# Kernel tuning notes

Measured on AMD Instinct MI355X. Metric: run time of the kernel, lower is better.

Reference implementation:

```python
import jax, jax.numpy as jnp
import numpy as np

N_NODES = 32768
N_EDGES = 131072
BATCH = 512
SEQ_LEN = 1000
VOCAB = 26  # vocab_size=25 + 1 padding row
EMB = 128


def _bn(x, g, b):
    # BatchNorm1d forward with batch statistics (training-mode math), eps=1e-5
    m = x.mean(0)
    v = x.var(0)
    return g * (x - m) * jax.lax.rsqrt(v + 1e-5) + b


def _gcn(x, src, dst, W, b, n):
    deg = 1.0 + jax.ops.segment_sum(jnp.ones(src.shape[0], x.dtype), dst, num_segments=n)
    dis = jax.lax.rsqrt(deg)
    xw = x @ W
    msg = xw[src] * (dis[src] * dis[dst])[:, None]
    agg = jax.ops.segment_sum(msg, dst, num_segments=n) + xw * (dis * dis)[:, None]
    return agg + b


def _conv1d(x, k, b, pad):
    # x: [B, C_in, L], k: [C_out, C_in, K]
    y = jax.lax.conv_general_dilated(x, k, (1,), [(pad, pad)],
                                     dimension_numbers=('NCH', 'OIH', 'NCH'))
    return y + b[None, :, None]


def setup_inputs() -> dict:
    key = jax.random.key(0)
    ks = jax.random.split(key, 32)
    f = lambda i, shape, s=0.1: (jax.random.normal(ks[i], shape, dtype=jnp.float32) * s)
    inp = {
        'x': jax.random.normal(ks[0], (N_NODES, 5), dtype=jnp.float32),
        'edge_index': jax.random.randint(ks[1], (2, N_EDGES), 0, N_NODES, dtype=jnp.int32),
        'batch': jnp.sort(jax.random.randint(ks[2], (N_NODES,), 0, BATCH, dtype=jnp.int32)),
        'protein_seq': jax.random.randint(ks[3], (BATCH, SEQ_LEN), 0, VOCAB, dtype=jnp.int32),
        # GCN weights
        'W1': f(4, (5, 64)), 'b1': f(5, (64,)),
        'g1': jnp.ones((64,)), 'bt1': jnp.zeros((64,)),
        'W2': f(6, (64, 128)), 'b2': f(7, (128,)),
        'g2': jnp.ones((128,)), 'bt2': jnp.zeros((128,)),
        'W3': f(8, (128, 128)), 'b3': f(9, (128,)),
        'g3': jnp.ones((128,)), 'bt3': jnp.zeros((128,)),
        # protein embedding (row 0 = padding_idx, zeroed)
        'emb': f(10, (VOCAB, EMB)).at[0].set(0.0),
        # protein convs
        'ck1': f(11, (32, 128, 4)), 'cb1': f(12, (32,)),
        'ck2': f(13, (64, 32, 6)), 'cb2': f(14, (64,)),
        'ck3': f(15, (96, 64, 8)), 'cb3': f(16, (96,)),
        'fw1': f(17, (224, 512)), 'fb1': f(18, (512,)),
        'fw2': f(19, (512, 256)), 'fb2': f(20, (256,)),
        'fw3': f(21, (256, 1)), 'fb3': f(22, (1,)),
    }
    return inp


def reference(x, edge_index, batch, protein_seq,
              W1, b1, g1, bt1, W2, b2, g2, bt2, W3, b3, g3, bt3,
              emb, ck1, cb1, ck2, cb2, ck3, cb3,
              fw1, fb1, fw2, fb2, fw3, fb3):
    src, dst = edge_index[0], edge_index[1]
    relu = jax.nn.relu
    # Drug GNN encoder
    h = relu(_bn(_gcn(x, src, dst, W1, b1, N_NODES), g1, bt1))
    h = relu(_bn(_gcn(h, src, dst, W2, b2, N_NODES), g2, bt2))
    h = relu(_bn(_gcn(h, src, dst, W3, b3, N_NODES), g3, bt3))
    cnt = jax.ops.segment_sum(jnp.ones(N_NODES, h.dtype), batch, num_segments=BATCH)
    drug_emb = jax.ops.segment_sum(h, batch, num_segments=BATCH) / jnp.maximum(cnt, 1.0)[:, None]
    # Protein CNN encoder
    e = emb[protein_seq]                    # [B, L, 128]
    p = jnp.transpose(e, (0, 2, 1))         # [B, 128, L]
    p = relu(_conv1d(p, ck1, cb1, 1))       # [B, 32, 999]
    p = relu(_conv1d(p, ck2, cb2, 2))       # [B, 64, 998]
    p = relu(_conv1d(p, ck3, cb3, 3))       # [B, 96, 997]
    prot_emb = p.max(axis=2)                # [B, 96]
    c = jnp.concatenate([drug_emb, prot_emb], axis=1)  # [B, 224]
    c = relu(c @ fw1 + fb1)
    c = relu(c @ fw2 + fb2)
    out = (c @ fw3 + fb3)[:, 0]             # [B]
    return out
```

## Files before the change

kernel.cpp:

```cpp
#include <hip/hip_runtime.h>

#define NN 32768
#define NE 131072
#define NB 512
#define SL 1000

using bf16x8 = __attribute__((ext_vector_type(8))) short;
using f32x4  = __attribute__((ext_vector_type(4))) float;

static __device__ __forceinline__ unsigned short f2b(float f) {
  union { float f; unsigned u; } x; x.f = f;
  unsigned r = x.u + 0x7fffu + ((x.u >> 16) & 1u);
  return (unsigned short)(r >> 16);
}

static __device__ __forceinline__ void bn_from_raw(float sum, float ssq, float g, float b,
                                                   float& sc, float& sh) {
  float m = sum / 32768.f;
  float v = ssq / 32768.f - m * m;
  sc = g * rsqrtf(v + 1e-5f);
  sh = b - m * sc;
}

__global__ void k_degprep(const int* __restrict__ dst, int* __restrict__ degi,
// ... 192 lines not shown
      acc[t].x += a.y * w1.x; acc[t].y += a.y * w1.y; acc[t].z += a.y * w1.z; acc[t].w += a.y * w1.w;
      acc[t].x += a.z * w2.x; acc[t].y += a.z * w2.y; acc[t].z += a.z * w2.z; acc[t].w += a.z * w2.w;
      acc[t].x += a.w * w3.x; acc[t].y += a.w * w3.y; acc[t].z += a.w * w3.z; acc[t].w += a.w * w3.w;
    }
  }
  float4 s4 = {0.f, 0.f, 0.f, 0.f}, ss4 = {0.f, 0.f, 0.f, 0.f};
#pragma unroll
  for (int t = 0; t < TN; ++t) {
    float4 o = acc[t];
    if (RELU) {
      o.x = fmaxf(o.x, 0.f); o.y = fmaxf(o.y, 0.f);
      o.z = fmaxf(o.z, 0.f); o.w = fmaxf(o.w, 0.f);
    }
    *(float4*)&out[(n0 + t) * C_OUT + co] = o;
    if (STATS) {
      s4.x += o.x; s4.y += o.y; s4.z += o.z; s4.w += o.w;
      ss4.x += o.x * o.x; ss4.y += o.y * o.y;
      ss4.z += o.z * o.z; ss4.w += o.w * o.w;
    }
  }
  if (STATS) {
    __shared__ float red2[GPB][C_OUT];
    int grp = threadIdx.x / CO4;
    *(float4*)&red2[grp][co] = s4;
    __syncthreads();
    if (threadIdx.x < C_OUT) {
      float t = 0.f;
#pragma unroll
      for (int s = 0; s < GPB; ++s) t += red2[s][threadIdx.x];
      atomicAdd(&st[threadIdx.x], t);
    }
    __syncthreads();
    *(float4*)&red2[grp][co] = ss4;
    __syncthreads();
    if (threadIdx.x < C_OUT) {
      float t = 0.f;
#pragma unroll
      for (int s = 0; s < GPB; ++s) t += red2[s][threadIdx.x];
      atomicAdd(&st[C_OUT + threadIdx.x], t);
    }
  }
}

__launch_bounds__(256)
__global__ void k_reg(const float* __restrict__ cbuf,
                      const float* __restrict__ fw1, const float* __restrict__ fb1,
                      const float* __restrict__ fw2, const float* __restrict__ fb2,
                      const float* __restrict__ fw3, const float* __restrict__ fb3,
                      float* __restrict__ out) {
  __shared__ float cin[224];
  __shared__ float h1[512];
  __shared__ float h2[256];
  __shared__ float red[4];
  int b = blockIdx.x, t = threadIdx.x;
  if (t < 224) cin[t] = cbuf[b * 224 + t];
  __syncthreads();
  {
    float a0 = fb1[t], a1 = fb1[t + 256];
    for (int ci = 0; ci < 224; ++ci) {
      float av = cin[ci];
      a0 += av * fw1[ci * 512 + t];
      a1 += av * fw1[ci * 512 + t + 256];
    }
    h1[t] = fmaxf(a0, 0.f);
    h1[t + 256] = fmaxf(a1, 0.f);
  }
  __syncthreads();
  {
    float a = fb2[t];
    for (int ci = 0; ci < 512; ++ci) a += h1[ci] * fw2[ci * 256 + t];
    h2[t] = fmaxf(a, 0.f);
  }
  __syncthreads();
  {
    float p = h2[t] * fw3[t];
#pragma unroll
    for (int off = 32; off > 0; off >>= 1) p += __shfl_down(p, off, 64);
    if ((t & 63) == 0) red[t >> 6] = p;
    __syncthreads();
    if (t == 0) out[b] = red[0] + red[1] + red[2] + red[3] + fb3[0];
  }
}

__launch_bounds__(256, 3)
__global__ void conv_mfma(const int* __restrict__ seq, const unsigned short* __restrict__ emb_bf,
                          const unsigned short* __restrict__ wt1g, const float* __restrict__ cb1,
                          const unsigned short* __restrict__ wt2g, const float* __restrict__ cb2,
                          const unsigned short* __restrict__ wt3g, const float* __restrict__ cb3,
                          const float* __restrict__ agg, const float* __restrict__ st3,
                          const float* __restrict__ g3, const float* __restrict__ bt3,
                          const int* __restrict__ batch, float* __restrict__ outmax) {
  __shared__ __align__(16) unsigned short s_w[12288];
  __shared__ __align__(16) unsigned short s_c1[4864];
  __shared__ __align__(16) unsigned short s_c2[9216];
  __shared__ int s_tok[152];
  __shared__ int s_max[96];

  int tid = threadIdx.x;
  int b = blockIdx.y;

  if (blockIdx.x == 8) {
    __shared__ int s_lo, s_hi;
    if (tid == 0) {
      int lo = 0, hi = NN;
      while (lo < hi) { int m = (lo + hi) >> 1; if (batch[m] < b) lo = m + 1; else hi = m; }
      s_lo = lo;
      hi = NN;
      while (lo < hi) { int m = (lo + hi) >> 1; if (batch[m] <= b) lo = m + 1; else hi = m; }
      s_hi = lo;
    }
    __syncthreads();
    if (tid < 128) {
      int lo = s_lo, hi = s_hi, c = tid;
      float sc, sh;
      bn_from_raw(st3[c], st3[128 + c], g3[c], bt3[c], sc, sh);
      float s = 0.f;
      for (int n = lo; n < hi; ++n) s += fmaxf(agg[(long)n * 128 + c] * sc + sh, 0.f);
      outmax[b * 224 + c] = s / fmaxf((float)(hi - lo), 1.0f);
    }
    return;
  }

  int t0 = blockIdx.x * 128;

  if (tid < 96) s_max[tid] = 0;
  if (tid < 152) {
    int p = t0 - 6 + tid;
    s_tok[tid] = (p >= 0 && p < SL) ? seq[b * SL + p] : 0;
  }
  if (tid < 128) ((int*)(s_c1 + 144 * 32))[tid] = 0;

  {
    int v0 = tid, v1 = tid + 256;
    *(bf16x8*)&s_w[(v0 >> 4) * 128 + ((((v0 >> 4) ^ v0) & 15) << 3)] = *(const bf16x8*)(wt1g + v0 * 8);
    *(bf16x8*)&s_w[(v1 >> 4) * 128 + ((((v1 >> 4) ^ v1) & 15) << 3)] = *(const bf16x8*)(wt1g + v1 * 8);
  }
  __syncthreads();

  int lane = tid & 63, wave = tid >> 6;
  int l15 = lane & 15, quad = lane >> 4;

  {
    int mt0 = wave, mt1 = wave + 4;
    f32x4 acc0[2], acc1[2], acc2[2];
#pragma unroll
    for (int nt = 0; nt < 2; ++nt) {
      float bv = cb1[nt * 16 + l15];
      acc0[nt] = (f32x4){bv, bv, bv, bv};
      acc1[nt] = (f32x4){bv, bv, bv, bv};
      acc2[nt] = (f32x4){bv, bv, bv, bv};
    }
    for (int kt = 0; kt < 4; ++kt) {
      int bo = (kt & 1) * 4096;
      if (kt < 3) {
        int bo2 = 4096 - bo;
        const unsigned short* wsrc = wt1g + (kt + 1) * 4096;
        int v0 = tid, v1 = tid + 256;
        *(bf16x8*)&s_w[bo2 + (v0 >> 4) * 128 + ((((v0 >> 4) ^ v0) & 15) << 3)] = *(const bf16x8*)(wsrc + v0 * 8);
        *(bf16x8*)&s_w[bo2 + (v1 >> 4) * 128 + ((((v1 >> 4) ^ v1) & 15) << 3)] = *(const bf16x8*)(wsrc + v1 * 8);
      }
      const unsigned short* e0 = emb_bf + s_tok[mt0 * 16 + l15 + kt] * 128 + quad * 8;
      const unsigned short* e1 = emb_bf + s_tok[mt1 * 16 + l15 + kt] * 128 + quad * 8;
#pragma unroll
      for (int cb = 0; cb < 4; ++cb) {
        bf16x8 a0 = *(const bf16x8*)(e0 + cb * 32);
        bf16x8 a1 = *(const bf16x8*)(e1 + cb * 32);
#pragma unroll
        for (int nt = 0; nt < 2; ++nt) {
          bf16x8 bf = *(const bf16x8*)&s_w[bo + (nt * 16 + l15) * 128 + (((cb * 4 + quad) ^ l15) << 3)];
          acc0[nt] = __builtin_amdgcn_mfma_f32_16x16x32_bf16(a0, bf, acc0[nt], 0, 0, 0);
          acc1[nt] = __builtin_amdgcn_mfma_f32_16x16x32_bf16(a1, bf, acc1[nt], 0, 0, 0);
        }
      }
      if (wave == 0) {
        const unsigned short* e2 = emb_bf + s_tok[128 + l15 + kt] * 128 + quad * 8;
#pragma unroll
        for (int cb = 0; cb < 4; ++cb) {
          bf16x8 a2 = *(const bf16x8*)(e2 + cb * 32);
#pragma unroll
          for (int nt = 0; nt < 2; ++nt) {
            bf16x8 bf = *(const bf16x8*)&s_w[bo + (nt * 16 + l15) * 128 + (((cb * 4 + quad) ^ l15) << 3)];
            acc2[nt] = __builtin_amdgcn_mfma_f32_16x16x32_bf16(a2, bf, acc2[nt], 0, 0, 0);
          }
        }
      }
      __syncthreads();
    }
#pragma unroll
    for (int nt = 0; nt < 2; ++nt) {
      int co = nt * 16 + l15;
#pragma unroll
      for (int r = 0; r < 4; ++r) {
        {
          int m = mt0 * 16 + quad * 4 + r;
          int l1 = t0 - 5 + m;
          unsigned short hv = f2b(fmaxf(acc0[nt][r], 0.f));
          s_c1[m * 32 + ((((co >> 3) ^ m) & 3) << 3) + (co & 7)] = (l1 >= 0 && l1 < 999) ? hv : (unsigned short)0;
        }
        {
          int m = mt1 * 16 + quad * 4 + r;
          int l1 = t0 - 5 + m;
          unsigned short hv = f2b(fmaxf(acc1[nt][r], 0.f));
          s_c1[m * 32 + ((((co >> 3) ^ m) & 3) << 3) + (co & 7)] = (l1 >= 0 && l1 < 999) ? hv : (unsigned short)0;
        }
      }
    }
    if (wave == 0) {
#pragma unroll
      for (int nt = 0; nt < 2; ++nt) {
        int co = nt * 16 + l15;
#pragma unroll
        for (int r = 0; r < 4; ++r) {
          int m = 128 + quad * 4 + r;
          int l1 = t0 - 5 + m;
          unsigned short hv = f2b(fmaxf(acc2[nt][r], 0.f));
          s_c1[m * 32 + ((((co >> 3) ^ m) & 3) << 3) + (co & 7)] = (l1 >= 0 && l1 < 999) ? hv : (unsigned short)0;
        }
      }
    }
  }

  {
    bf16x8 w2t[6];
#pragma unroll
    for (int c = 0; c < 6; ++c) w2t[c] = *(const bf16x8*)(wt2g + (c * 256 + tid) * 8);
#pragma unroll
    for (int c = 0; c < 6; ++c) {
      int ch = c * 256 + tid;
      int row = ch >> 2;
      *(bf16x8*)&s_w[row * 32 + (((row ^ ch) & 3) << 3)] = w2t[c];
    }
    __syncthreads();
  }

  {
    int mt0 = wave, mt1 = wave + 4;
    f32x4 acc[2][4];
#pragma unroll
    for (int nt = 0; nt < 4; ++nt) {
      float bv = cb2[nt * 16 + l15];
      acc[0][nt] = (f32x4){bv, bv, bv, bv};
      acc[1][nt] = (f32x4){bv, bv, bv, bv};
    }
    for (int kt = 0; kt < 6; ++kt) {
      int r0 = mt0 * 16 + l15 + kt, r1 = mt1 * 16 + l15 + kt;
      bf16x8 a0 = *(const bf16x8*)&s_c1[r0 * 32 + (((quad ^ r0) & 3) << 3)];
      bf16x8 a1 = *(const bf16x8*)&s_c1[r1 * 32 + (((quad ^ r1) & 3) << 3)];
#pragma unroll
      for (int nt = 0; nt < 4; ++nt) {
        int wr = kt * 64 + nt * 16 + l15;
        bf16x8 bf = *(const bf16x8*)&s_w[wr * 32 + (((quad ^ wr) & 3) << 3)];
        acc[0][nt] = __builtin_amdgcn_mfma_f32_16x16x32_bf16(a0, bf, acc[0][nt], 0, 0, 0);
        acc[1][nt] = __builtin_amdgcn_mfma_f32_16x16x32_bf16(a1, bf, acc[1][nt], 0, 0, 0);
      }
    }
#pragma unroll
    for (int mb = 0; mb < 2; ++mb) {
      int mt = mb ? mt1 : mt0;
#pragma unroll
      for (int nt = 0; nt < 4; ++nt) {
        int co = nt * 16 + l15;
#pragma unroll
        for (int r = 0; r < 4; ++r) {
          int m = mt * 16 + quad * 4 + r;
          int l2 = t0 - 3 + m;
          unsigned short hv = f2b(fmaxf(acc[mb][nt][r], 0.f));
          s_c2[m * 64 + ((((co >> 3) ^ m) & 7) << 3) + (co & 7)] = (l2 >= 0 && l2 < 998) ? hv : (unsigned short)0;
        }
      }
    }
    if (wave == 0) {
      f32x4 acc8[4];
#pragma unroll
      for (int nt = 0; nt < 4; ++nt) {
        float bv = cb2[nt * 16 + l15];
        acc8[nt] = (f32x4){bv, bv, bv, bv};
      }
      for (int kt = 0; kt < 6; ++kt) {
        int r0 = 128 + l15 + kt;
        bf16x8 a0 = *(const bf16x8*)&s_c1[r0 * 32 + (((quad ^ r0) & 3) << 3)];
#pragma unroll
        for (int nt = 0; nt < 4; ++nt) {
          int wr = kt * 64 + nt * 16 + l15;
          bf16x8 bf = *(const bf16x8*)&s_w[wr * 32 + (((quad ^ wr) & 3) << 3)];
          acc8[nt] = __builtin_amdgcn_mfma_f32_16x16x32_bf16(a0, bf, acc8[nt], 0, 0, 0);
        }
      }
#pragma unroll
      for (int nt = 0; nt < 4; ++nt) {
        int co = nt * 16 + l15;
#pragma unroll
        for (int r = 0; r < 4; ++r) {
          int m = 128 + quad * 4 + r;
          int l2 = t0 - 3 + m;
          unsigned short hv = f2b(fmaxf(acc8[nt][r], 0.f));
          s_c2[m * 64 + ((((co >> 3) ^ m) & 7) << 3) + (co & 7)] = (l2 >= 0 && l2 < 998) ? hv : (unsigned short)0;
        }
      }
    }
  }

  {
    bf16x8 w3t[3];
#pragma unroll
    for (int c = 0; c < 3; ++c) w3t[c] = *(const bf16x8*)(wt3g + (c * 256 + tid) * 8);
    __syncthreads();
#pragma unroll
    for (int c = 0; c < 3; ++c) {
      int ch = c * 256 + tid;
      int row = ch >> 3;
      *(bf16x8*)&s_w[row * 64 + (((row ^ ch) & 7) << 3)] = w3t[c];
    }
    __syncthreads();
  }

  {
    int mt0 = wave, mt1 = wave + 4;
    f32x4 acc[2][6];
#pragma unroll
    for (int nt = 0; nt < 6; ++nt) {
      float bv = cb3[nt * 16 + l15];
      acc[0][nt] = (f32x4){bv, bv, bv, bv};
      acc[1][nt] = (f32x4){bv, bv, bv, bv};
    }
    for (int kt = 0; kt < 8; ++kt) {
      bf16x8 w3t[3];
      if (kt < 7) {
#pragma unroll
        for (int c = 0; c < 3; ++c)
          w3t[c] = *(const bf16x8*)(wt3g + ((kt + 1) * 768 + c * 256 + tid) * 8);
      }
      int bo = (kt & 1) * 6144;
      int ra0 = mt0 * 16 + l15 + kt, ra1 = mt1 * 16 + l15 + kt;
#pragma unroll
      for (int cb = 0; cb < 2; ++cb) {
        bf16x8 a0 = *(const bf16x8*)&s_c2[ra0 * 64 + ((((cb * 4 + quad) ^ ra0) & 7) << 3)];
        bf16x8 a1 = *(const bf16x8*)&s_c2[ra1 * 64 + ((((cb * 4 + quad) ^ ra1) & 7) << 3)];
#pragma unroll
        for (int nt = 0; nt < 6; ++nt) {
          int wr = nt * 16 + l15;
          bf16x8 bf = *(const bf16x8*)&s_w[bo + wr * 64 + ((((cb * 4 + quad) ^ wr) & 7) << 3)];
          acc[0][nt] = __builtin_amdgcn_mfma_f32_16x16x32_bf16(a0, bf, acc[0][nt], 0, 0, 0);
          acc[1][nt] = __builtin_amdgcn_mfma_f32_16x16x32_bf16(a1, bf, acc[1][nt], 0, 0, 0);
        }
      }
      if (kt < 7) {
        int bo2 = 6144 - bo;
#pragma unroll
        for (int c = 0; c < 3; ++c) {
          int ch = c * 256 + tid;
          int row = ch >> 3;
          *(bf16x8*)&s_w[bo2 + row * 64 + (((row ^ ch) & 7) << 3)] = w3t[c];
        }
      }
      __syncthreads();
    }
#pragma unroll
    for (int nt = 0; nt < 6; ++nt) {
      int co = nt * 16 + l15;
      float mx = 0.f;
#pragma unroll
      for (int mb = 0; mb < 2; ++mb) {
        int mt = mb ? mt1 : mt0;
#pragma unroll
        for (int r = 0; r < 4; ++r) {
          int l3 = t0 + mt * 16 + quad * 4 + r;
          if (l3 < 997) mx = fmaxf(mx, acc[mb][nt][r]);
        }
      }
      atomicMax(&s_max[co], __float_as_int(mx));
    }
  }
  __syncthreads();
  if (tid < 96) atomicMax((int*)&outmax[b * 224 + 128 + tid], s_max[tid]);
}

extern "C" void kernel_launch(void* const* d_in, const int* in_sizes, int n_in,
                              void* d_out, int out_size, void* d_ws, size_t ws_size,
                              hipStream_t stream) {
  (void)in_sizes; (void)n_in; (void)out_size; (void)ws_size;
  const float* x = (const float*)d_in[0];
  const int* ei = (const int*)d_in[1];
  const int* batch = (const int*)d_in[2];
  const int* seq = (const int*)d_in[3];
  const float* W1 = (const float*)d_in[4];
  const float* g1 = (const float*)d_in[6];
  const float* bt1 = (const float*)d_in[7];
  const float* W2 = (const float*)d_in[8];
  const float* g2 = (const float*)d_in[10];
  const float* bt2 = (const float*)d_in[11];
  const float* W3 = (const float*)d_in[12];
  const float* g3 = (const float*)d_in[14];
  const float* bt3 = (const float*)d_in[15];
  const float* emb = (const float*)d_in[16];
  const float* ck1 = (const float*)d_in[17];
  const float* cb1 = (const float*)d_in[18];
  const float* ck2 = (const float*)d_in[19];
  const float* cb2 = (const float*)d_in[20];
  const float* ck3 = (const float*)d_in[21];
  const float* cb3 = (const float*)d_in[22];
  const float* fw1 = (const float*)d_in[23];
  const float* fb1 = (const float*)d_in[24];
  const float* fw2 = (const float*)d_in[25];
  const float* fb2 = (const float*)d_in[26];
  const float* fw3 = (const float*)d_in[27];
  const float* fb3 = (const float*)d_in[28];
  const int* src = ei;
  const int* dst = ei + NE;

  float* ws = (float*)d_ws;
  float* bufA = ws;
  float* bufB = ws + 4194304;
  float* dis = ws + 8388608;
  float* stats = ws + 8421376;
  float* cbuf = ws + 8422032;
  int* degi = (int*)(ws + 8536720);
  int* base = degi + NN;
  int* cursor = base + NN + 1;
  unsigned short* csr_src = (unsigned short*)(cursor + NN);
  unsigned short* emb_bf = (unsigned short*)(ws + 8700564);
  unsigned short* wt1 = emb_bf + 3328;
  unsigned short* wt2 = wt1 + 16384;
  unsigned short* wt3 = wt2 + 12288;
  float* out = (float*)d_out;

  hipMemsetAsync(stats, 0, (656 + 114688 + 32768) * sizeof(float), stream);

  k_degprep<<<NE / 256, 256, 0, stream>>>(dst, degi, emb, ck1, ck2, ck3, emb_bf, wt1, wt2, wt3);
  k_scan<<<1, 1024, 0, stream>>>(degi, base, cursor, dis);
  k_fill<<<NE / 256, 256, 0, stream>>>(src, dst, cursor, csr_src, NE);

  k_gfc1s<<<NN / 256, 256, 0, stream>>>(x, dis, base, csr_src, W1, bufA, stats);
  k_gbngather<64><<<NN * 16 / 256, 256, 0, stream>>>(bufA, dis, base, csr_src, stats, g1, bt1, bufB);
  k_fc4<128, 64, 4, false, false, true><<<1024, 256, 0, stream>>>(bufB, W2, nullptr, bufA, stats + 128, NN);
  k_gbngather<128><<<NN * 32 / 256, 256, 0, stream>>>(bufA, dis, base, csr_src, stats + 128, g2, bt2, bufB);
  k_fc4<128, 128, 4, false, false, true><<<1024, 256, 0, stream>>>(bufB, W3, nullptr, bufA, stats + 384, NN);

  conv_mfma<<<dim3(9, NB), 256, 0, stream>>>(seq, emb_bf, wt1, cb1, wt2, cb2, wt3, cb3,
                                             bufA, stats + 384, g3, bt3, batch, cbuf);

  k_reg<<<NB, 256, 0, stream>>>(cbuf, fw1, fb1, fw2, fb2, fw3, fb3, out);
}
```

Before: 431.2 us.

## Read conv weights directly from global memory instead of staging in LDS

Removes the 24 KB shared weight buffer and its double-buffered staging for all three conv layers, so MFMA B operands are loaded straight from global or L2 memory. This drops many __syncthreads and LDS writes, and the smaller LDS footprint lets launch bounds rise to 4 blocks per CU. The cost is more global-load latency inside the MFMA loops, since the weight reads now depend on cache hits, and possible register pressure under the tighter occupancy bound.

```diff
diff --git a/kernel.cpp b/kernel.cpp
--- a/kernel.cpp
+++ b/kernel.cpp
@@ -298,7 +298,7 @@
   }
 }
 
-__launch_bounds__(256, 3)
+__launch_bounds__(256, 4)
 __global__ void conv_mfma(const int* __restrict__ seq, const unsigned short* __restrict__ emb_bf,
                           const unsigned short* __restrict__ wt1g, const float* __restrict__ cb1,
                           const unsigned short* __restrict__ wt2g, const float* __restrict__ cb2,
@@ -306,7 +306,6 @@
                           const float* __restrict__ agg, const float* __restrict__ st3,
                           const float* __restrict__ g3, const float* __restrict__ bt3,
                           const int* __restrict__ batch, float* __restrict__ outmax) {
-  __shared__ __align__(16) unsigned short s_w[12288];
   __shared__ __align__(16) unsigned short s_c1[4864];
   __shared__ __align__(16) unsigned short s_c2[9216];
   __shared__ int s_tok[152];
@@ -345,12 +344,6 @@
     s_tok[tid] = (p >= 0 && p < SL) ? seq[b * SL + p] : 0;
   }
   if (tid < 128) ((int*)(s_c1 + 144 * 32))[tid] = 0;
-
-  {
-    int v0 = tid, v1 = tid + 256;
-    *(bf16x8*)&s_w[(v0 >> 4) * 128 + ((((v0 >> 4) ^ v0) & 15) << 3)] = *(const bf16x8*)(wt1g + v0 * 8);
-    *(bf16x8*)&s_w[(v1 >> 4) * 128 + ((((v1 >> 4) ^ v1) & 15) << 3)] = *(const bf16x8*)(wt1g + v1 * 8);
-  }
   __syncthreads();
 
   int lane = tid & 63, wave = tid >> 6;
@@ -367,23 +360,16 @@
       acc2[nt] = (f32x4){bv, bv, bv, bv};
     }
     for (int kt = 0; kt < 4; ++kt) {
-      int bo = (kt & 1) * 4096;
-      if (kt < 3) {
-        int bo2 = 4096 - bo;
-        const unsigned short* wsrc = wt1g + (kt + 1) * 4096;
-        int v0 = tid, v1 = tid + 256;
-        *(bf16x8*)&s_w[bo2 + (v0 >> 4) * 128 + ((((v0 >> 4) ^ v0) & 15) << 3)] = *(const bf16x8*)(wsrc + v0 * 8);
-        *(bf16x8*)&s_w[bo2 + (v1 >> 4) * 128 + ((((v1 >> 4) ^ v1) & 15) << 3)] = *(const bf16x8*)(wsrc + v1 * 8);
-      }
       const unsigned short* e0 = emb_bf + s_tok[mt0 * 16 + l15 + kt] * 128 + quad * 8;
       const unsigned short* e1 = emb_bf + s_tok[mt1 * 16 + l15 + kt] * 128 + quad * 8;
+      const unsigned short* wb = wt1g + kt * 4096 + l15 * 128 + quad * 8;
 #pragma unroll
       for (int cb = 0; cb < 4; ++cb) {
         bf16x8 a0 = *(const bf16x8*)(e0 + cb * 32);
         bf16x8 a1 = *(const bf16x8*)(e1 + cb * 32);
 #pragma unroll
         for (int nt = 0; nt < 2; ++nt) {
-          bf16x8 bf = *(const bf16x8*)&s_w[bo + (nt * 16 + l15) * 128 + (((cb * 4 + quad) ^ l15) << 3)];
+          bf16x8 bf = *(const bf16x8*)(wb + nt * 2048 + cb * 32);
           acc0[nt] = __builtin_amdgcn_mfma_f32_16x16x32_bf16(a0, bf, acc0[nt], 0, 0, 0);
           acc1[nt] = __builtin_amdgcn_mfma_f32_16x16x32_bf16(a1, bf, acc1[nt], 0, 0, 0);
         }
@@ -395,12 +381,11 @@
           bf16x8 a2 = *(const bf16x8*)(e2 + cb * 32);
 #pragma unroll
           for (int nt = 0; nt < 2; ++nt) {
-            bf16x8 bf = *(const bf16x8*)&s_w[bo + (nt * 16 + l15) * 128 + (((cb * 4 + quad) ^ l15) << 3)];
+            bf16x8 bf = *(const bf16x8*)(wb + nt * 2048 + cb * 32);
             acc2[nt] = __builtin_amdgcn_mfma_f32_16x16x32_bf16(a2, bf, acc2[nt], 0, 0, 0);
           }
         }
       }
-      __syncthreads();
     }
 #pragma unroll
     for (int nt = 0; nt < 2; ++nt) {
@@ -435,19 +420,7 @@
       }
     }
   }
-
-  {
-    bf16x8 w2t[6];
-#pragma unroll
-    for (int c = 0; c < 6; ++c) w2t[c] = *(const bf16x8*)(wt2g + (c * 256 + tid) * 8);
-#pragma unroll
-    for (int c = 0; c < 6; ++c) {
-      int ch = c * 256 + tid;
-      int row = ch >> 2;
-      *(bf16x8*)&s_w[row * 32 + (((row ^ ch) & 3) << 3)] = w2t[c];
-    }
-    __syncthreads();
-  }
+  __syncthreads();
 
   {
     int mt0 = wave, mt1 = wave + 4;
@@ -462,10 +435,10 @@
       int r0 = mt0 * 16 + l15 + kt, r1 = mt1 * 16 + l15 + kt;
       bf16x8 a0 = *(const bf16x8*)&s_c1[r0 * 32 + (((quad ^ r0) & 3) << 3)];
       bf16x8 a1 = *(const bf16x8*)&s_c1[r1 * 32 + (((quad ^ r1) & 3) << 3)];
+      const unsigned short* wb = wt2g + kt * 2048 + l15 * 32 + quad * 8;
 #pragma unroll
       for (int nt = 0; nt < 4; ++nt) {
-        int wr = kt * 64 + nt * 16 + l15;
-        bf16x8 bf = *(const bf16x8*)&s_w[wr * 32 + (((quad ^ wr) & 3) << 3)];
+        bf16x8 bf = *(const bf16x8*)(wb + nt * 512);
         acc[0][nt] = __builtin_amdgcn_mfma_f32_16x16x32_bf16(a0, bf, acc[0][nt], 0, 0, 0);
         acc[1][nt] = __builtin_amdgcn_mfma_f32_16x16x32_bf16(a1, bf, acc[1][nt], 0, 0, 0);
       }
@@ -495,10 +468,10 @@
       for (int kt = 0; kt < 6; ++kt) {
         int r0 = 128 + l15 + kt;
         bf16x8 a0 = *(const bf16x8*)&s_c1[r0 * 32 + (((quad ^ r0) & 3) << 3)];
+        const unsigned short* wb = wt2g + kt * 2048 + l15 * 32 + quad * 8;
 #pragma unroll
         for (int nt = 0; nt < 4; ++nt) {
-          int wr = kt * 64 + nt * 16 + l15;
-          bf16x8 bf = *(const bf16x8*)&s_w[wr * 32 + (((quad ^ wr) & 3) << 3)];
+          bf16x8 bf = *(const bf16x8*)(wb + nt * 512);
           acc8[nt] = __builtin_amdgcn_mfma_f32_16x16x32_bf16(a0, bf, acc8[nt], 0, 0, 0);
         }
       }
@@ -515,20 +488,7 @@
       }
     }
   }
-
-  {
-    bf16x8 w3t[3];
-#pragma unroll
-    for (int c = 0; c < 3; ++c) w3t[c] = *(const bf16x8*)(wt3g + (c * 256 + tid) * 8);
-    __syncthreads();
-#pragma unroll
-    for (int c = 0; c < 3; ++c) {
-      int ch = c * 256 + tid;
-      int row = ch >> 3;
-      *(bf16x8*)&s_w[row * 64 + (((row ^ ch) & 7) << 3)] = w3t[c];
-    }
-    __syncthreads();
-  }
+  __syncthreads();
 
   {
     int mt0 = wave, mt1 = wave + 4;
@@ -540,36 +500,19 @@
       acc[1][nt] = (f32x4){bv, bv, bv, bv};
     }
     for (int kt = 0; kt < 8; ++kt) {
-      bf16x8 w3t[3];
-      if (kt < 7) {
-#pragma unroll
-        for (int c = 0; c < 3; ++c)
-          w3t[c] = *(const bf16x8*)(wt3g + ((kt + 1) * 768 + c * 256 + tid) * 8);
-      }
-      int bo = (kt & 1) * 6144;
       int ra0 = mt0 * 16 + l15 + kt, ra1 = mt1 * 16 + l15 + kt;
+      const unsigned short* wb = wt3g + kt * 6144 + l15 * 64 + quad * 8;
 #pragma unroll
       for (int cb = 0; cb < 2; ++cb) {
         bf16x8 a0 = *(const bf16x8*)&s_c2[ra0 * 64 + ((((cb * 4 + quad) ^ ra0) & 7) << 3)];
         bf16x8 a1 = *(const bf16x8*)&s_c2[ra1 * 64 + ((((cb * 4 + quad) ^ ra1) & 7) << 3)];
 #pragma unroll
         for (int nt = 0; nt < 6; ++nt) {
-          int wr = nt * 16 + l15;
-          bf16x8 bf = *(const bf16x8*)&s_w[bo + wr * 64 + ((((cb * 4 + quad) ^ wr) & 7) << 3)];
+          bf16x8 bf = *(const bf16x8*)(wb + nt * 1024 + cb * 32);
           acc[0][nt] = __builtin_amdgcn_mfma_f32_16x16x32_bf16(a0, bf, acc[0][nt], 0, 0, 0);
           acc[1][nt] = __builtin_amdgcn_mfma_f32_16x16x32_bf16(a1, bf, acc[1][nt], 0, 0, 0);
         }
       }
-      if (kt < 7) {
-        int bo2 = 6144 - bo;
-#pragma unroll
-        for (int c = 0; c < 3; ++c) {
-          int ch = c * 256 + tid;
-          int row = ch >> 3;
-          *(bf16x8*)&s_w[bo2 + row * 64 + (((row ^ ch) & 7) << 3)] = w3t[c];
-        }
-      }
-      __syncthreads();
     }
 #pragma unroll
     for (int nt = 0; nt < 6; ++nt) {
```

New measurement: 637.6 us. 1.48x slower.

## Use 512-thread blocks in conv kernel with one M-tile per wave

Applied to the files above, without the earlier changes.

The fused protein conv kernel now runs with 8 waves per block instead of 4. Each wave handles a single 16-row M tile rather than two, and the weight-staging loops are reindexed for 512 threads. The goal is more wave-level parallelism per block and fewer accumulator registers per thread, which should help hide latency. The cost is less reuse of each weight fragment loaded from LDS, since every B fragment now feeds one MFMA instead of two. Barriers also span more waves.

```diff
diff --git a/kernel.cpp b/kernel.cpp
--- a/kernel.cpp
+++ b/kernel.cpp
@@ -298,7 +298,7 @@
   }
 }
 
-__launch_bounds__(256, 3)
+__launch_bounds__(512, 6)
 __global__ void conv_mfma(const int* __restrict__ seq, const unsigned short* __restrict__ emb_bf,
                           const unsigned short* __restrict__ wt1g, const float* __restrict__ cb1,
                           const unsigned short* __restrict__ wt2g, const float* __restrict__ cb2,
@@ -347,9 +347,8 @@
   if (tid < 128) ((int*)(s_c1 + 144 * 32))[tid] = 0;
 
   {
-    int v0 = tid, v1 = tid + 256;
+    int v0 = tid;
     *(bf16x8*)&s_w[(v0 >> 4) * 128 + ((((v0 >> 4) ^ v0) & 15) << 3)] = *(const bf16x8*)(wt1g + v0 * 8);
-    *(bf16x8*)&s_w[(v1 >> 4) * 128 + ((((v1 >> 4) ^ v1) & 15) << 3)] = *(const bf16x8*)(wt1g + v1 * 8);
   }
   __syncthreads();
 
@@ -357,13 +356,12 @@
   int l15 = lane & 15, quad = lane >> 4;
 
   {
-    int mt0 = wave, mt1 = wave + 4;
-    f32x4 acc0[2], acc1[2], acc2[2];
+    int mt0 = wave;
+    f32x4 acc0[2], acc2[2];
 #pragma unroll
     for (int nt = 0; nt < 2; ++nt) {
       float bv = cb1[nt * 16 + l15];
       acc0[nt] = (f32x4){bv, bv, bv, bv};
-      acc1[nt] = (f32x4){bv, bv, bv, bv};
       acc2[nt] = (f32x4){bv, bv, bv, bv};
     }
     for (int kt = 0; kt < 4; ++kt) {
@@ -371,21 +369,17 @@
       if (kt < 3) {
         int bo2 = 4096 - bo;
         const unsigned short* wsrc = wt1g + (kt + 1) * 4096;
-        int v0 = tid, v1 = tid + 256;
+        int v0 = tid;
         *(bf16x8*)&s_w[bo2 + (v0 >> 4) * 128 + ((((v0 >> 4) ^ v0) & 15) << 3)] = *(const bf16x8*)(wsrc + v0 * 8);
-        *(bf16x8*)&s_w[bo2 + (v1 >> 4) * 128 + ((((v1 >> 4) ^ v1) & 15) << 3)] = *(const bf16x8*)(wsrc + v1 * 8);
       }
       const unsigned short* e0 = emb_bf + s_tok[mt0 * 16 + l15 + kt] * 128 + quad * 8;
-      const unsigned short* e1 = emb_bf + s_tok[mt1 * 16 + l15 + kt] * 128 + quad * 8;
 #pragma unroll
       for (int cb = 0; cb < 4; ++cb) {
         bf16x8 a0 = *(const bf16x8*)(e0 + cb * 32);
-        bf16x8 a1 = *(const bf16x8*)(e1 + cb * 32);
 #pragma unroll
         for (int nt = 0; nt < 2; ++nt) {
           bf16x8 bf = *(const bf16x8*)&s_w[bo + (nt * 16 + l15) * 128 + (((cb * 4 + quad) ^ l15) << 3)];
           acc0[nt] = __builtin_amdgcn_mfma_f32_16x16x32_bf16(a0, bf, acc0[nt], 0, 0, 0);
-          acc1[nt] = __builtin_amdgcn_mfma_f32_16x16x32_bf16(a1, bf, acc1[nt], 0, 0, 0);
         }
       }
       if (wave == 0) {
@@ -407,18 +401,10 @@
       int co = nt * 16 + l15;
 #pragma unroll
       for (int r = 0; r < 4; ++r) {
-        {
-          int m = mt0 * 16 + quad * 4 + r;
-          int l1 = t0 - 5 + m;
-          unsigned short hv = f2b(fmaxf(acc0[nt][r], 0.f));
-          s_c1[m * 32 + ((((co >> 3) ^ m) & 3) << 3) + (co & 7)] = (l1 >= 0 && l1 < 999) ? hv : (unsigned short)0;
-        }
-        {
-          int m = mt1 * 16 + quad * 4 + r;
-          int l1 = t0 - 5 + m;
-          unsigned short hv = f2b(fmaxf(acc1[nt][r], 0.f));
-          s_c1[m * 32 + ((((co >> 3) ^ m) & 3) << 3) + (co & 7)] = (l1 >= 0 && l1 < 999) ? hv : (unsigned short)0;
-        }
+        int m = mt0 * 16 + quad * 4 + r;
+        int l1 = t0 - 5 + m;
+        unsigned short hv = f2b(fmaxf(acc0[nt][r], 0.f));
+        s_c1[m * 32 + ((((co >> 3) ^ m) & 3) << 3) + (co & 7)] = (l1 >= 0 && l1 < 999) ? hv : (unsigned short)0;
       }
     }
     if (wave == 0) {
@@ -437,12 +423,12 @@
   }
 
   {
-    bf16x8 w2t[6];
-#pragma unroll
-    for (int c = 0; c < 6; ++c) w2t[c] = *(const bf16x8*)(wt2g + (c * 256 + tid) * 8);
-#pragma unroll
-    for (int c = 0; c < 6; ++c) {
-      int ch = c * 256 + tid;
+    bf16x8 w2t[3];
+#pragma unroll
+    for (int c = 0; c < 3; ++c) w2t[c] = *(const bf16x8*)(wt2g + (c * 512 + tid) * 8);
+#pragma unroll
+    for (int c = 0; c < 3; ++c) {
+      int ch = c * 512 + tid;
       int row = ch >> 2;
       *(bf16x8*)&s_w[row * 32 + (((row ^ ch) & 3) << 3)] = w2t[c];
     }
@@ -450,58 +436,46 @@
   }
 
   {
-    int mt0 = wave, mt1 = wave + 4;
-    f32x4 acc[2][4];
+    int mt0 = wave;
+    f32x4 acc[4], acc8[4];
 #pragma unroll
     for (int nt = 0; nt < 4; ++nt) {
       float bv = cb2[nt * 16 + l15];
-      acc[0][nt] = (f32x4){bv, bv, bv, bv};
-      acc[1][nt] = (f32x4){bv, bv, bv, bv};
+      acc[nt] = (f32x4){bv, bv, bv, bv};
+      acc8[nt] = (f32x4){bv, bv, bv, bv};
     }
     for (int kt = 0; kt < 6; ++kt) {
-      int r0 = mt0 * 16 + l15 + kt, r1 = mt1 * 16 + l15 + kt;
+      int r0 = mt0 * 16 + l15 + kt;
       bf16x8 a0 = *(const bf16x8*)&s_c1[r0 * 32 + (((quad ^ r0) & 3) << 3)];
-      bf16x8 a1 = *(const bf16x8*)&s_c1[r1 * 32 + (((quad ^ r1) & 3) << 3)];
 #pragma unroll
       for (int nt = 0; nt < 4; ++nt) {
         int wr = kt * 64 + nt * 16 + l15;
         bf16x8 bf = *(const bf16x8*)&s_w[wr * 32 + (((quad ^ wr) & 3) << 3)];
-        acc[0][nt] = __builtin_amdgcn_mfma_f32_16x16x32_bf16(a0, bf, acc[0][nt], 0, 0, 0);
-        acc[1][nt] = __builtin_amdgcn_mfma_f32_16x16x32_bf16(a1, bf, acc[1][nt], 0, 0, 0);
-      }
-    }
-#pragma unroll
-    for (int mb = 0; mb < 2; ++mb) {
-      int mt = mb ? mt1 : mt0;
-#pragma unroll
-      for (int nt = 0; nt < 4; ++nt) {
-        int co = nt * 16 + l15;
-#pragma unroll
-        for (int r = 0; r < 4; ++r) {
-          int m = mt * 16 + quad * 4 + r;
-          int l2 = t0 - 3 + m;
-          unsigned short hv = f2b(fmaxf(acc[mb][nt][r], 0.f));
-          s_c2[m * 64 + ((((co >> 3) ^ m) & 7) << 3) + (co & 7)] = (l2 >= 0 && l2 < 998) ? hv : (unsigned short)0;
-        }
-      }
-    }
-    if (wave == 0) {
-      f32x4 acc8[4];
-#pragma unroll
-      for (int nt = 0; nt < 4; ++nt) {
-        float bv = cb2[nt * 16 + l15];
-        acc8[nt] = (f32x4){bv, bv, bv, bv};
-      }
-      for (int kt = 0; kt < 6; ++kt) {
-        int r0 = 128 + l15 + kt;
-        bf16x8 a0 = *(const bf16x8*)&s_c1[r0 * 32 + (((quad ^ r0) & 3) << 3)];
+        acc[nt] = __builtin_amdgcn_mfma_f32_16x16x32_bf16(a0, bf, acc[nt], 0, 0, 0);
+      }
+      if (wave == 0) {
+        int r8 = 128 + l15 + kt;
+        bf16x8 a8 = *(const bf16x8*)&s_c1[r8 * 32 + (((quad ^ r8) & 3) << 3)];
 #pragma unroll
         for (int nt = 0; nt < 4; ++nt) {
           int wr = kt * 64 + nt * 16 + l15;
           bf16x8 bf = *(const bf16x8*)&s_w[wr * 32 + (((quad ^ wr) & 3) << 3)];
-          acc8[nt] = __builtin_amdgcn_mfma_f32_16x16x32_bf16(a0, bf, acc8[nt], 0, 0, 0);
-        }
-      }
+          acc8[nt] = __builtin_amdgcn_mfma_f32_16x16x32_bf16(a8, bf, acc8[nt], 0, 0, 0);
+        }
+      }
+    }
+#pragma unroll
+    for (int nt = 0; nt < 4; ++nt) {
+      int co = nt * 16 + l15;
+#pragma unroll
+      for (int r = 0; r < 4; ++r) {
+        int m = mt0 * 16 + quad * 4 + r;
+        int l2 = t0 - 3 + m;
+        unsigned short hv = f2b(fmaxf(acc[nt][r], 0.f));
+        s_c2[m * 64 + ((((co >> 3) ^ m) & 7) << 3) + (co & 7)] = (l2 >= 0 && l2 < 998) ? hv : (unsigned short)0;
+      }
+    }
+    if (wave == 0) {
 #pragma unroll
       for (int nt = 0; nt < 4; ++nt) {
         int co = nt * 16 + l15;
@@ -517,56 +491,56 @@
   }
 
   {
-    bf16x8 w3t[3];
-#pragma unroll
-    for (int c = 0; c < 3; ++c) w3t[c] = *(const bf16x8*)(wt3g + (c * 256 + tid) * 8);
-    __syncthreads();
-#pragma unroll
-    for (int c = 0; c < 3; ++c) {
-      int ch = c * 256 + tid;
-      int row = ch >> 3;
-      *(bf16x8*)&s_w[row * 64 + (((row ^ ch) & 7) << 3)] = w3t[c];
-    }
-    __syncthreads();
-  }
-
-  {
-    int mt0 = wave, mt1 = wave + 4;
-    f32x4 acc[2][6];
+    bf16x8 w3t0, w3t1;
+    w3t0 = *(const bf16x8*)(wt3g + tid * 8);
+    if (tid < 256) w3t1 = *(const bf16x8*)(wt3g + (512 + tid) * 8);
+    __syncthreads();
+    {
+      int ch = tid, row = ch >> 3;
+      *(bf16x8*)&s_w[row * 64 + (((row ^ ch) & 7) << 3)] = w3t0;
+    }
+    if (tid < 256) {
+      int ch = 512 + tid, row = ch >> 3;
+      *(bf16x8*)&s_w[row * 64 + (((row ^ ch) & 7) << 3)] = w3t1;
+    }
+    __syncthreads();
+  }
+
+  {
+    int mt0 = wave;
+    f32x4 acc[6];
 #pragma unroll
     for (int nt = 0; nt < 6; ++nt) {
       float bv = cb3[nt * 16 + l15];
-      acc[0][nt] = (f32x4){bv, bv, bv, bv};
-      acc[1][nt] = (f32x4){bv, bv, bv, bv};
+      acc[nt] = (f32x4){bv, bv, bv, bv};
     }
     for (int kt = 0; kt < 8; ++kt) {
-      bf16x8 w3t[3];
+      bf16x8 w3t0, w3t1;
       if (kt < 7) {
-#pragma unroll
-        for (int c = 0; c < 3; ++c)
-          w3t[c] = *(const bf16x8*)(wt3g + ((kt + 1) * 768 + c * 256 + tid) * 8);
+        w3t0 = *(const bf16x8*)(wt3g + ((kt + 1) * 768 + tid) * 8);
+        if (tid < 256) w3t1 = *(const bf16x8*)(wt3g + ((kt + 1) * 768 + 512 + tid) * 8);
       }
       int bo = (kt & 1) * 6144;
-      int ra0 = mt0 * 16 + l15 + kt, ra1 = mt1 * 16 + l15 + kt;
+      int ra0 = mt0 * 16 + l15 + kt;
 #pragma unroll
       for (int cb = 0; cb < 2; ++cb) {
         bf16x8 a0 = *(const bf16x8*)&s_c2[ra0 * 64 + ((((cb * 4 + quad) ^ ra0) & 7) << 3)];
-        bf16x8 a1 = *(const bf16x8*)&s_c2[ra1 * 64 + ((((cb * 4 + quad) ^ ra1) & 7) << 3)];
 #pragma unroll
         for (int nt = 0; nt < 6; ++nt) {
           int wr = nt * 16 + l15;
           bf16x8 bf = *(const bf16x8*)&s_w[bo + wr * 64 + ((((cb * 4 + quad) ^ wr) & 7) << 3)];
-          acc[0][nt] = __builtin_amdgcn_mfma_f32_16x16x32_bf16(a0, bf, acc[0][nt], 0, 0, 0);
-          acc[1][nt] = __builtin_amdgcn_mfma_f32_16x16x32_bf16(a1, bf, acc[1][nt], 0, 0, 0);
+          acc[nt] = __builtin_amdgcn_mfma_f32_16x16x32_bf16(a0, bf, acc[nt], 0, 0, 0);
         }
       }
       if (kt < 7) {
         int bo2 = 6144 - bo;
-#pragma unroll
-        for (int c = 0; c < 3; ++c) {
-          int ch = c * 256 + tid;
-          int row = ch >> 3;
-          *(bf16x8*)&s_w[bo2 + row * 64 + (((row ^ ch) & 7) << 3)] = w3t[c];
+        {
+          int ch = tid, row = ch >> 3;
+          *(bf16x8*)&s_w[bo2 + row * 64 + (((row ^ ch) & 7) << 3)] = w3t0;
+        }
+        if (tid < 256) {
+          int ch = 512 + tid, row = ch >> 3;
+          *(bf16x8*)&s_w[bo2 + row * 64 + (((row ^ ch) & 7) << 3)] = w3t1;
         }
       }
       __syncthreads();
@@ -576,13 +550,9 @@
       int co = nt * 16 + l15;
       float mx = 0.f;
 #pragma unroll
-      for (int mb = 0; mb < 2; ++mb) {
-        int mt = mb ? mt1 : mt0;
-#pragma unroll
-        for (int r = 0; r < 4; ++r) {
-          int l3 = t0 + mt * 16 + quad * 4 + r;
-          if (l3 < 997) mx = fmaxf(mx, acc[mb][nt][r]);
-        }
+      for (int r = 0; r < 4; ++r) {
+        int l3 = t0 + mt0 * 16 + quad * 4 + r;
+        if (l3 < 997) mx = fmaxf(mx, acc[nt][r]);
       }
       atomicMax(&s_max[co], __float_as_int(mx));
     }
@@ -652,7 +622,7 @@
   k_gbngather<128><<<NN * 32 / 256, 256, 0, stream>>>(bufA, dis, base, csr_src, stats + 128, g2, bt2, bufB);
   k_fc4<128, 128, 4, false, false, true><<<1024, 256, 0, stream>>>(bufB, W3, nullptr, bufA, stats + 384, NN);
 
-  conv_mfma<<<dim3(9, NB), 256, 0, stream>>>(seq, emb_bf, wt1, cb1, wt2, cb2, wt3, cb3,
+  conv_mfma<<<dim3(9, NB), 512, 0, stream>>>(seq, emb_bf, wt1, cb1, wt2, cb2, wt3, cb3,
                                              bufA, stats + 384, g3, bt3, batch, cbuf);
 
   k_reg<<<NB, 256, 0, stream>>>(cbuf, fw1, fb1, fw2, fb2, fw3, fb3, out);
```

New measurement: 431.6 us. About the same (+0.1%).

## Process two proteins per 512-thread block sharing conv weight tiles in LDS

Applied to the files above, without the earlier changes.

The conv kernel now runs 512-thread blocks that each handle two batch elements. Both halves share one set of staged weight tiles in LDS while keeping separate token, intermediate and max buffers. This halves the number of global-to-LDS weight loads and the per-block staging work per protein. In exchange LDS use per block rises, s_c2 is trimmed to 136 rows with a bounds guard, and launch bounds change to (512,4), which may tighten the register budget.

```diff
diff --git a/kernel.cpp b/kernel.cpp
--- a/kernel.cpp
+++ b/kernel.cpp
@@ -298,7 +298,7 @@
   }
 }
 
-__launch_bounds__(256, 3)
+__launch_bounds__(512, 4)
 __global__ void conv_mfma(const int* __restrict__ seq, const unsigned short* __restrict__ emb_bf,
                           const unsigned short* __restrict__ wt1g, const float* __restrict__ cb1,
                           const unsigned short* __restrict__ wt2g, const float* __restrict__ cb2,
@@ -307,57 +307,68 @@
                           const float* __restrict__ g3, const float* __restrict__ bt3,
                           const int* __restrict__ batch, float* __restrict__ outmax) {
   __shared__ __align__(16) unsigned short s_w[12288];
-  __shared__ __align__(16) unsigned short s_c1[4864];
-  __shared__ __align__(16) unsigned short s_c2[9216];
-  __shared__ int s_tok[152];
-  __shared__ int s_max[96];
+  __shared__ __align__(16) unsigned short s_c1[2][4864];
+  __shared__ __align__(16) unsigned short s_c2[2][8704];
+  __shared__ int s_tok[2][152];
+  __shared__ int s_max[2][96];
 
   int tid = threadIdx.x;
-  int b = blockIdx.y;
+  int by = blockIdx.y;
 
   if (blockIdx.x == 8) {
-    __shared__ int s_lo, s_hi;
-    if (tid == 0) {
+    __shared__ int s_lo[2], s_hi[2];
+    if (tid == 0 || tid == 128) {
+      int g = tid >> 7;
+      int bb = 2 * by + g;
       int lo = 0, hi = NN;
-      while (lo < hi) { int m = (lo + hi) >> 1; if (batch[m] < b) lo = m + 1; else hi = m; }
-      s_lo = lo;
+      while (lo < hi) { int m = (lo + hi) >> 1; if (batch[m] < bb) lo = m + 1; else hi = m; }
+      s_lo[g] = lo;
       hi = NN;
-      while (lo < hi) { int m = (lo + hi) >> 1; if (batch[m] <= b) lo = m + 1; else hi = m; }
-      s_hi = lo;
-    }
-    __syncthreads();
-    if (tid < 128) {
-      int lo = s_lo, hi = s_hi, c = tid;
+      while (lo < hi) { int m = (lo + hi) >> 1; if (batch[m] <= bb) lo = m + 1; else hi = m; }
+      s_hi[g] = lo;
+    }
+    __syncthreads();
+    if (tid < 256) {
+      int g = tid >> 7, c = tid & 127;
+      int bb = 2 * by + g;
+      int lo = s_lo[g], hi = s_hi[g];
       float sc, sh;
       bn_from_raw(st3[c], st3[128 + c], g3[c], bt3[c], sc, sh);
       float s = 0.f;
       for (int n = lo; n < hi; ++n) s += fmaxf(agg[(long)n * 128 + c] * sc + sh, 0.f);
-      outmax[b * 224 + c] = s / fmaxf((float)(hi - lo), 1.0f);
+      outmax[bb * 224 + c] = s / fmaxf((float)(hi - lo), 1.0f);
     }
     return;
   }
 
   int t0 = blockIdx.x * 128;
 
-  if (tid < 96) s_max[tid] = 0;
+  if (tid < 192) ((int*)s_max)[tid] = 0;
   if (tid < 152) {
     int p = t0 - 6 + tid;
-    s_tok[tid] = (p >= 0 && p < SL) ? seq[b * SL + p] : 0;
-  }
-  if (tid < 128) ((int*)(s_c1 + 144 * 32))[tid] = 0;
-
-  {
-    int v0 = tid, v1 = tid + 256;
+    s_tok[0][tid] = (p >= 0 && p < SL) ? seq[(2 * by) * SL + p] : 0;
+  } else if (tid >= 256 && tid < 408) {
+    int p = t0 - 6 + (tid - 256);
+    s_tok[1][tid - 256] = (p >= 0 && p < SL) ? seq[(2 * by + 1) * SL + p] : 0;
+  }
+  if ((tid & 255) < 128) ((int*)&s_c1[tid >> 8][144 * 32])[tid & 127] = 0;
+
+  {
+    int v0 = tid;
     *(bf16x8*)&s_w[(v0 >> 4) * 128 + ((((v0 >> 4) ^ v0) & 15) << 3)] = *(const bf16x8*)(wt1g + v0 * 8);
-    *(bf16x8*)&s_w[(v1 >> 4) * 128 + ((((v1 >> 4) ^ v1) & 15) << 3)] = *(const bf16x8*)(wt1g + v1 * 8);
-  }
-  __syncthreads();
-
-  int lane = tid & 63, wave = tid >> 6;
+  }
+  __syncthreads();
+
+  int wg = tid >> 8;
+  int ltid = tid & 255;
+  int lane = ltid & 63, wv = ltid >> 6;
   int l15 = lane & 15, quad = lane >> 4;
-
-  {
-    int mt0 = wave, mt1 = wave + 4;
+  const int* tok = s_tok[wg];
+  unsigned short* c1 = s_c1[wg];
+  unsigned short* c2 = s_c2[wg];
+
+  {
+    int mt0 = wv, mt1 = wv + 4;
     f32x4 acc0[2], acc1[2], acc2[2];
 #pragma unroll
     for (int nt = 0; nt < 2; ++nt) {
@@ -371,12 +382,11 @@
       if (kt < 3) {
         int bo2 = 4096 - bo;
         const unsigned short* wsrc = wt1g + (kt + 1) * 4096;
-        int v0 = tid, v1 = tid + 256;
+        int v0 = tid;
         *(bf16x8*)&s_w[bo2 + (v0 >> 4) * 128 + ((((v0 >> 4) ^ v0) & 15) << 3)] = *(const bf16x8*)(wsrc + v0 * 8);
-        *(bf16x8*)&s_w[bo2 + (v1 >> 4) * 128 + ((((v1 >> 4) ^ v1) & 15) << 3)] = *(const bf16x8*)(wsrc + v1 * 8);
-      }
-      const unsigned short* e0 = emb_bf + s_tok[mt0 * 16 + l15 + kt] * 128 + quad * 8;
-      const unsigned short* e1 = emb_bf + s_tok[mt1 * 16 + l15 + kt] * 128 + quad * 8;
+      }
+      const unsigned short* e0 = emb_bf + tok[mt0 * 16 + l15 + kt] * 128 + quad * 8;
+      const unsigned short* e1 = emb_bf + tok[mt1 * 16 + l15 + kt] * 128 + quad * 8;
 #pragma unroll
       for (int cb = 0; cb < 4; ++cb) {
         bf16x8 a0 = *(const bf16x8*)(e0 + cb * 32);
@@ -388,8 +398,8 @@
           acc1[nt] = __builtin_amdgcn_mfma_f32_16x16x32_bf16(a1, bf, acc1[nt], 0, 0, 0);
         }
       }
-      if (wave == 0) {
-        const unsigned short* e2 = emb_bf + s_tok[128 + l15 + kt] * 128 + quad * 8;
+      if (wv == 0) {
+        const unsigned short* e2 = emb_bf + tok[128 + l15 + kt] * 128 + quad * 8;
 #pragma unroll
         for (int cb = 0; cb < 4; ++cb) {
           bf16x8 a2 = *(const bf16x8*)(e2 + cb * 32);
@@ -411,17 +421,17 @@
           int m = mt0 * 16 + quad * 4 + r;
           int l1 = t0 - 5 + m;
           unsigned short hv = f2b(fmaxf(acc0[nt][r], 0.f));
-          s_c1[m * 32 + ((((co >> 3) ^ m) & 3) << 3) + (co & 7)] = (l1 >= 0 && l1 < 999) ? hv : (unsigned short)0;
+          c1[m * 32 + ((((co >> 3) ^ m) & 3) << 3) + (co & 7)] = (l1 >= 0 && l1 < 999) ? hv : (unsigned short)0;
         }
         {
           int m = mt1 * 16 + quad * 4 + r;
           int l1 = t0 - 5 + m;
           unsigned short hv = f2b(fmaxf(acc1[nt][r], 0.f));
-          s_c1[m * 32 + ((((co >> 3) ^ m) & 3) << 3) + (co & 7)] = (l1 >= 0 && l1 < 999) ? hv : (unsigned short)0;
-        }
-      }
-    }
-    if (wave == 0) {
+          c1[m * 32 + ((((co >> 3) ^ m) & 3) << 3) + (co & 7)] = (l1 >= 0 && l1 < 999) ? hv : (unsigned short)0;
+        }
+      }
+    }
+    if (wv == 0) {
 #pragma unroll
       for (int nt = 0; nt < 2; ++nt) {
         int co = nt * 16 + l15;
@@ -430,19 +440,19 @@
           int m = 128 + quad * 4 + r;
           int l1 = t0 - 5 + m;
           unsigned short hv = f2b(fmaxf(acc2[nt][r], 0.f));
-          s_c1[m * 32 + ((((co >> 3) ^ m) & 3) << 3) + (co & 7)] = (l1 >= 0 && l1 < 999) ? hv : (unsigned short)0;
-        }
-      }
-    }
-  }
-
-  {
-    bf16x8 w2t[6];
-#pragma unroll
-    for (int c = 0; c < 6; ++c) w2t[c] = *(const bf16x8*)(wt2g + (c * 256 + tid) * 8);
-#pragma unroll
-    for (int c = 0; c < 6; ++c) {
-      int ch = c * 256 + tid;
+          c1[m * 32 + ((((co >> 3) ^ m) & 3) << 3) + (co & 7)] = (l1 >= 0 && l1 < 999) ? hv : (unsigned short)0;
+        }
+      }
+    }
+  }
+
+  {
+    bf16x8 w2t[3];
+#pragma unroll
+    for (int c = 0; c < 3; ++c) w2t[c] = *(const bf16x8*)(wt2g + (c * 512 + tid) * 8);
+#pragma unroll
+    for (int c = 0; c < 3; ++c) {
+      int ch = c * 512 + tid;
       int row = ch >> 2;
       *(bf16x8*)&s_w[row * 32 + (((row ^ ch) & 3) << 3)] = w2t[c];
     }
@@ -450,7 +460,7 @@
   }
 
   {
-    int mt0 = wave, mt1 = wave + 4;
+    int mt0 = wv, mt1 = wv + 4;
     f32x4 acc[2][4];
 #pragma unroll
     for (int nt = 0; nt < 4; ++nt) {
@@ -460,8 +470,8 @@
     }
     for (int kt = 0; kt < 6; ++kt) {
       int r0 = mt0 * 16 + l15 + kt, r1 = mt1 * 16 + l15 + kt;
-      bf16x8 a0 = *(const bf16x8*)&s_c1[r0 * 32 + (((quad ^ r0) & 3) << 3)];
-      bf16x8 a1 = *(const bf16x8*)&s_c1[r1 * 32 + (((quad ^ r1) & 3) << 3)];
+      bf16x8 a0 = *(const bf16x8*)&c1[r0 * 32 + (((quad ^ r0) & 3) << 3)];
+      bf16x8 a1 = *(const bf16x8*)&c1[r1 * 32 + (((quad ^ r1) & 3) << 3)];
 #pragma unroll
       for (int nt = 0; nt < 4; ++nt) {
         int wr = kt * 64 + nt * 16 + l15;
@@ -481,11 +491,11 @@
           int m = mt * 16 + quad * 4 + r;
           int l2 = t0 - 3 + m;
           unsigned short hv = f2b(fmaxf(acc[mb][nt][r], 0.f));
-          s_c2[m * 64 + ((((co >> 3) ^ m) & 7) << 3) + (co & 7)] = (l2 >= 0 && l2 < 998) ? hv : (unsigned short)0;
-        }
-      }
-    }
-    if (wave == 0) {
+          c2[m * 64 + ((((co >> 3) ^ m) & 7) << 3) + (co & 7)] = (l2 >= 0 && l2 < 998) ? hv : (unsigned short)0;
+        }
+      }
+    }
+    if (wv == 0) {
       f32x4 acc8[4];
 #pragma unroll
       for (int nt = 0; nt < 4; ++nt) {
@@ -494,7 +504,7 @@
       }
       for (int kt = 0; kt < 6; ++kt) {
         int r0 = 128 + l15 + kt;
-        bf16x8 a0 = *(const bf16x8*)&s_c1[r0 * 32 + (((quad ^ r0) & 3) << 3)];
+        bf16x8 a0 = *(const bf16x8*)&c1[r0 * 32 + (((quad ^ r0) & 3) << 3)];
 #pragma unroll
         for (int nt = 0; nt < 4; ++nt) {
           int wr = kt * 64 + nt * 16 + l15;
@@ -510,28 +520,31 @@
           int m = 128 + quad * 4 + r;
           int l2 = t0 - 3 + m;
           unsigned short hv = f2b(fmaxf(acc8[nt][r], 0.f));
-          s_c2[m * 64 + ((((co >> 3) ^ m) & 7) << 3) + (co & 7)] = (l2 >= 0 && l2 < 998) ? hv : (unsigned short)0;
-        }
-      }
-    }
-  }
-
-  {
-    bf16x8 w3t[3];
-#pragma unroll
-    for (int c = 0; c < 3; ++c) w3t[c] = *(const bf16x8*)(wt3g + (c * 256 + tid) * 8);
-    __syncthreads();
-#pragma unroll
-    for (int c = 0; c < 3; ++c) {
-      int ch = c * 256 + tid;
-      int row = ch >> 3;
-      *(bf16x8*)&s_w[row * 64 + (((row ^ ch) & 7) << 3)] = w3t[c];
-    }
-    __syncthreads();
-  }
-
-  {
-    int mt0 = wave, mt1 = wave + 4;
+          if (m < 136)
+            c2[m * 64 + ((((co >> 3) ^ m) & 7) << 3) + (co & 7)] = (l2 >= 0 && l2 < 998) ? hv : (unsigned short)0;
+        }
+      }
+    }
+  }
+
+  {
+    bf16x8 w3t0, w3t1;
+    w3t0 = *(const bf16x8*)(wt3g + tid * 8);
+    if (tid < 256) w3t1 = *(const bf16x8*)(wt3g + (512 + tid) * 8);
+    __syncthreads();
+    {
+      int ch = tid, row = ch >> 3;
+      *(bf16x8*)&s_w[row * 64 + (((row ^ ch) & 7) << 3)] = w3t0;
+    }
+    if (tid < 256) {
+      int ch = 512 + tid, row = ch >> 3;
+      *(bf16x8*)&s_w[row * 64 + (((row ^ ch) & 7) << 3)] = w3t1;
+    }
+    __syncthreads();
+  }
+
+  {
+    int mt0 = wv, mt1 = wv + 4;
     f32x4 acc[2][6];
 #pragma unroll
     for (int nt = 0; nt < 6; ++nt) {
@@ -540,18 +553,17 @@
       acc[1][nt] = (f32x4){bv, bv, bv, bv};
     }
     for (int kt = 0; kt < 8; ++kt) {
-      bf16x8 w3t[3];
+      bf16x8 w3t0, w3t1;
       if (kt < 7) {
-#pragma unroll
-        for (int c = 0; c < 3; ++c)
-          w3t[c] = *(const bf16x8*)(wt3g + ((kt + 1) * 768 + c * 256 + tid) * 8);
+        w3t0 = *(const bf16x8*)(wt3g + ((kt + 1) * 768 + tid) * 8);
+        if (tid < 256) w3t1 = *(const bf16x8*)(wt3g + ((kt + 1) * 768 + 512 + tid) * 8);
       }
       int bo = (kt & 1) * 6144;
       int ra0 = mt0 * 16 + l15 + kt, ra1 = mt1 * 16 + l15 + kt;
 #pragma unroll
       for (int cb = 0; cb < 2; ++cb) {
-        bf16x8 a0 = *(const bf16x8*)&s_c2[ra0 * 64 + ((((cb * 4 + quad) ^ ra0) & 7) << 3)];
-        bf16x8 a1 = *(const bf16x8*)&s_c2[ra1 * 64 + ((((cb * 4 + quad) ^ ra1) & 7) << 3)];
+        bf16x8 a0 = *(const bf16x8*)&c2[ra0 * 64 + ((((cb * 4 + quad) ^ ra0) & 7) << 3)];
+        bf16x8 a1 = *(const bf16x8*)&c2[ra1 * 64 + ((((cb * 4 + quad) ^ ra1) & 7) << 3)];
 #pragma unroll
         for (int nt = 0; nt < 6; ++nt) {
           int wr = nt * 16 + l15;
@@ -562,11 +574,13 @@
       }
       if (kt < 7) {
         int bo2 = 6144 - bo;
-#pragma unroll
-        for (int c = 0; c < 3; ++c) {
-          int ch = c * 256 + tid;
-          int row = ch >> 3;
-          *(bf16x8*)&s_w[bo2 + row * 64 + (((row ^ ch) & 7) << 3)] = w3t[c];
+        {
+          int ch = tid, row = ch >> 3;
+          *(bf16x8*)&s_w[bo2 + row * 64 + (((row ^ ch) & 7) << 3)] = w3t0;
+        }
+        if (tid < 256) {
+          int ch = 512 + tid, row = ch >> 3;
+          *(bf16x8*)&s_w[bo2 + row * 64 + (((row ^ ch) & 7) << 3)] = w3t1;
         }
       }
       __syncthreads();
@@ -584,11 +598,12 @@
           if (l3 < 997) mx = fmaxf(mx, acc[mb][nt][r]);
         }
       }
-      atomicMax(&s_max[co], __float_as_int(mx));
-    }
-  }
-  __syncthreads();
-  if (tid < 96) atomicMax((int*)&outmax[b * 224 + 128 + tid], s_max[tid]);
+      atomicMax(&s_max[wg][co], __float_as_int(mx));
+    }
+  }
+  __syncthreads();
+  if ((tid & 255) < 96)
+    atomicMax((int*)&outmax[(2 * by + (tid >> 8)) * 224 + 128 + (tid & 255)], s_max[tid >> 8][tid & 255]);
 }
 
 extern "C" void kernel_launch(void* const* d_in, const int* in_sizes, int n_in,
@@ -652,8 +667,8 @@
   k_gbngather<128><<<NN * 32 / 256, 256, 0, stream>>>(bufA, dis, base, csr_src, stats + 128, g2, bt2, bufB);
   k_fc4<128, 128, 4, false, false, true><<<1024, 256, 0, stream>>>(bufB, W3, nullptr, bufA, stats + 384, NN);
 
-  conv_mfma<<<dim3(9, NB), 256, 0, stream>>>(seq, emb_bf, wt1, cb1, wt2, cb2, wt3, cb3,
-                                             bufA, stats + 384, g3, bt3, batch, cbuf);
+  conv_mfma<<<dim3(9, NB / 2), 512, 0, stream>>>(seq, emb_bf, wt1, cb1, wt2, cb2, wt3, cb3,
+                                                 bufA, stats + 384, g3, bt3, batch, cbuf);
 
   k_reg<<<NB, 256, 0, stream>>>(cbuf, fw1, fb1, fw2, fb2, fw3, fb3, out);
 }
```

Result: no change. 434.2 us (+0.7%).
